# Performance work log

Hardware: AMD Instinct MI355X
Metric: run time of the kernel (lower is better)

The kernel has to match this reference:

```python
import jax, jax.numpy as jnp
import numpy as np
from jax import lax

B = 8192; LE = 40; LD = 12; PQ = 237; IN = PQ + 19; H = 64


def setup_inputs() -> dict:
    key = jax.random.key(0)
    ks = jax.random.split(key, 26)
    def n(k, shape, s=0.05):
        return jax.random.normal(k, shape, jnp.float32) * s
    return {
        "input_p_q": jax.random.normal(ks[0], (B, LE, PQ), jnp.float32),
        "label_p": jax.random.normal(ks[1], (B, LE), jnp.float32),
        "emb_hour": n(ks[2], (24, 5)),
        "emb_weekday": n(ks[3], (8, 3)),
        "emb_month": n(ks[4], (13, 4)),
        "emb_woy": n(ks[5], (54, 7)),
        "Wi_w": n(ks[6], (H, IN)), "Wi_b": n(ks[7], (H,)),
        "We_w": n(ks[8], (H, 2 * H)),
        "Vd_w": n(ks[9], (IN, H)), "Vd_b": n(ks[10], (IN,)),
        "enc_Wih": n(ks[11], (4 * H, IN)), "enc_Whh": n(ks[12], (4 * H, H)),
        "enc_bih": n(ks[13], (4 * H,)), "enc_bhh": n(ks[14], (4 * H,)),
        "Wd_w": n(ks[15], (H, H)), "Wd_b": n(ks[16], (H,)),
        "Wd2_w": n(ks[17], (H, 2)),
        "Vdt_w": n(ks[18], (1, H)), "Vdt_b": n(ks[19], (1,)),
        "dec_Wih": n(ks[20], (4, H + 1)), "dec_Whh": n(ks[21], (4, 1)),
        "dec_bih": n(ks[22], (4,)), "dec_bhh": n(ks[23], (4,)),
        "input_time": jax.random.randint(ks[24], (B, LE, 4), 0, 8),
        "decoder_time": jax.random.randint(ks[25], (B, LD), 0, 24),
    }


def _lstm_cell(x, h, c, Wih, Whh, bih, bhh):
    # PyTorch LSTMCell gate order: i, f, g, o
    g = x @ Wih.T + bih + h @ Whh.T + bhh
    i, f, gg, o = jnp.split(g, 4, axis=1)
    c = jax.nn.sigmoid(f) * c + jax.nn.sigmoid(i) * jnp.tanh(gg)
    h = jax.nn.sigmoid(o) * jnp.tanh(c)
    return h, c


def _forward(input_p_q, label_p, emb_hour, emb_weekday, emb_month, emb_woy,
             Wi_w, Wi_b, We_w, Vd_w, Vd_b,
             enc_Wih, enc_Whh, enc_bih, enc_bhh,
             Wd_w, Wd_b, Wd2_w, Vdt_w, Vdt_b,
             dec_Wih, dec_Whh, dec_bih, dec_bhh, input_time):
    b = input_p_q.shape[0]
    inputs = jnp.concatenate([
        input_p_q,
        emb_hour[input_time[:, :, 0]],
        emb_weekday[input_time[:, :, 1]],
        emb_month[input_time[:, :, 2]],
        emb_woy[input_time[:, :, 3]],
    ], axis=2)  # [B, LE, IN]

    def enc_step(carry, x_t):
        h, c = carry
        score = jnp.tanh(jnp.concatenate([h, c], 1) @ We_w.T
                         + x_t @ Wi_w.T + Wi_b) @ Vd_w.T + Vd_b  # [B, IN]
        x_in = x_t * jax.nn.softmax(score, axis=1)
        h, c = _lstm_cell(x_in, h, c, enc_Wih, enc_Whh, enc_bih, enc_bhh)
        return (h, c), h

    z = jnp.zeros((b, H), inputs.dtype)
    _, mid = lax.scan(enc_step, (z, z), jnp.swapaxes(inputs, 0, 1))
    mid_output = jnp.swapaxes(mid, 0, 1)  # [B, LE, H]

    wd_mid = mid_output @ Wd_w.T + Wd_b  # precompute Wd(mid_output), [B, LE, H]
    dec_p_in = label_p[:, LE - 1:LE]  # [B, 1], held constant across decode steps

    def dec_step(carry, _):
        hi, ci = carry  # [B, 1] each
        q = jnp.concatenate([hi, ci], 1) @ Wd2_w.T  # [B, H]
        score = jnp.tanh(q[:, None, :] + wd_mid) @ Vdt_w.T + Vdt_b  # [B, LE, 1] (no softmax, as in source)
        ctx = jnp.einsum('bt,btd->bd', score[..., 0], mid_output)  # [B, H]
        hi, ci = _lstm_cell(jnp.concatenate([ctx, dec_p_in], 1), hi, ci,
                            dec_Wih, dec_Whh, dec_bih, dec_bhh)
        return (hi, ci), hi

    z1 = jnp.zeros((b, 1), inputs.dtype)
    _, outs = lax.scan(dec_step, (z1, z1), None, length=LD)  # [LD, B, 1]
    return jnp.swapaxes(outs[..., 0], 0, 1)  # [B, LD]


def reference(input_p_q, label_p, emb_hour, emb_weekday, emb_month, emb_woy,
              Wi_w, Wi_b, We_w, Vd_w, Vd_b,
              enc_Wih, enc_Whh, enc_bih, enc_bhh,
              Wd_w, Wd_b, Wd2_w, Vdt_w, Vdt_b,
              dec_Wih, dec_Whh, dec_bih, dec_bhh, input_time, decoder_time):
    # decoder_time is accepted by the original forward but never used
    return _forward(input_p_q, label_p, emb_hour, emb_weekday, emb_month, emb_woy,
                    Wi_w, Wi_b, We_w, Vd_w, Vd_b,
                    enc_Wih, enc_Whh, enc_bih, enc_bhh,
                    Wd_w, Wd_b, Wd2_w, Vdt_w, Vdt_b,
                    dec_Wih, dec_Whh, dec_bih, dec_bhh, input_time)
```

## Files before the change

kernel.cpp:

```cpp
#include <hip/hip_runtime.h>

#define BB   8192
#define LEN  40
#define LDN  12
#define PQN  237
#define INN  256
#define HN   64
#define BT   32
#define ENC_BLOCKS (BB / BT)
#define DW   8
#define DEC_BLOCKS (BB / DW)
#define XPS  256

typedef unsigned int  u32;
typedef _Float16 f16;
typedef f16  half8 __attribute__((ext_vector_type(8)));
typedef f16  f16x4 __attribute__((ext_vector_type(4)));
typedef float f32x4 __attribute__((ext_vector_type(4)));

#define XS 264
#define HS 72

#define OFF_WI   0
#define OFF_WE   16384
#define OFF_VD   24576
#define OFF_WIH  40960
#define OFF_WHH  106496
#define OFF_WD   122880
#define W_TOTAL  126976

#define T_H   0
#define T_W   120
#define T_M   144
#define T_Y   196
#define T_TOT 574

#define PREP_BLOCKS (BB * LEN / 32)
#define CONV_BLOCKS ((W_TOTAL + 255) / 256)

__device__ __forceinline__ float rcp_(float x){
#if __has_builtin(__builtin_amdgcn_rcpf)
  return __builtin_amdgcn_rcpf(x);
#else
  return 1.0f / x;
#endif
}
__device__ __forceinline__ float sigm(float x){
  return rcp_(1.0f + exp2f(-1.44269504f * x));
}
__device__ __forceinline__ float tanhf_(float x){
  float e = exp2f(2.88539008f * x);
  return 1.0f - 2.0f * rcp_(e + 1.0f);
}

__device__ __forceinline__ void bar_lds(){
  asm volatile("s_waitcnt lgkmcnt(0)" ::: "memory");
  __builtin_amdgcn_s_barrier();
  asm volatile("" ::: "memory");
}

__global__ __launch_bounds__(256) void conv_w(
    const float* __restrict__ Wi, const float* __restrict__ We,
    const float* __restrict__ Vd, const float* __restrict__ Wih,
    const float* __restrict__ Whh, const float* __restrict__ Wd,
    f16* __restrict__ dst)
{
  int i = blockIdx.x * 256 + threadIdx.x;
  if (i >= W_TOTAL) return;
  float v;
  if      (i < OFF_WE)  v = Wi [i - OFF_WI ];
  else if (i < OFF_VD)  v = We [i - OFF_WE ];
  else if (i < OFF_WIH) v = Vd [i - OFF_VD ];
  else if (i < OFF_WHH) v = Wih[i - OFF_WIH];
  else if (i < OFF_WD)  v = Whh[i - OFF_WHH];
  else                  v = Wd [i - OFF_WD ];
  dst[i] = (f16)v;
}

__global__ __launch_bounds__(256) void prep_all(
    const float* __restrict__ ipq,
    const float* __restrict__ e_h, const float* __restrict__ e_w,
    const float* __restrict__ e_m, const float* __restrict__ e_y,
    const int*  __restrict__ itime,
    f16* __restrict__ xpre,
    const float* __restrict__ Wi, const float* __restrict__ We,
    const float* __restrict__ Vd, const float* __restrict__ Wih,
    const float* __restrict__ Whh, const float* __restrict__ Wd,
    f16* __restrict__ wdst)
{
  if (blockIdx.x >= PREP_BLOCKS) {
    int i = (blockIdx.x - PREP_BLOCKS) * 256 + threadIdx.x;
    if (i >= W_TOTAL) return;
    float v;
    if      (i < OFF_WE)  v = Wi [i - OFF_WI ];
    else if (i < OFF_VD)  v = We [i - OFF_WE ];
    else if (i < OFF_WIH) v = Vd [i - OFF_VD ];
    else if (i < OFF_WHH) v = Wih[i - OFF_WIH];
    else if (i < OFF_WD)  v = Whh[i - OFF_WHH];
    else                  v = Wd [i - OFF_WD ];
    wdst[i] = (f16)v;
    return;
  }
  const int wv = threadIdx.x >> 6, l = threadIdx.x & 63;
  const size_t row0 = (size_t)blockIdx.x * 32 + (size_t)wv * 8;
  int4 itv[8];
  #pragma unroll
  for (int r = 0; r < 8; ++r)
    itv[r] = *(const int4*)(itime + (row0 + r) * 4);
  #pragma unroll
  for (int r = 0; r < 8; ++r) {
    const size_t row = row0 + r;
    const float* src = ipq + row * PQN;
    f16* dst = xpre + row * XPS;
    #pragma unroll
    for (int k = 0; k < 3; ++k) {
      const int c = k * 64 + l;
      dst[c] = (f16)src[c];
    }
    {
      const int c = 192 + l;
      float v;
      if (c < PQN) v = src[c];
      else {
        const int o = c - PQN;
        if      (o < 5 ) v = e_h[itv[r].x * 5 + o];
        else if (o < 8 ) v = e_w[itv[r].y * 3 + (o - 5)];
        else if (o < 12) v = e_m[itv[r].z * 4 + (o - 8)];
        else             v = e_y[itv[r].w * 7 + (o - 12)];
      }
      dst[c] = (f16)v;
    }
  }
}

__global__ __launch_bounds__(512, 2) void enc_x(
    const f16* __restrict__ xpre,
    const float* __restrict__ Wi_b,
    const float* __restrict__ Vd_b,
    const float* __restrict__ ebih, const float* __restrict__ ebhh,
    const float* __restrict__ Wd_b,
    const f16*  __restrict__ wAll,
    f16* __restrict__ xout)
{
  __shared__ __attribute__((aligned(16))) f16 Xl[BT * XS];
  __shared__ __attribute__((aligned(16))) f16 Ul[BT * HS];
  __shared__ __attribute__((aligned(16))) f16 Hl[BT * HS];
  __shared__ __attribute__((aligned(16))) f16 Cl[BT * HS];
  __shared__ float Sred[2 * 64];
  __shared__ __attribute__((aligned(16))) f16 WiL[4 * 8 * 64 * 8];
  __shared__ __attribute__((aligned(16))) f16 WeL[4 * 4 * 64 * 8];
  __shared__ __attribute__((aligned(16))) f16 VdL[16 * 2 * 64 * 8];
  __shared__ __attribute__((aligned(16))) f16 WhL[16 * 2 * 64 * 8];
  __shared__ __attribute__((aligned(16))) f16 WdL[4 * 2 * 64 * 8];
  __shared__ float VdbL[256];
  __shared__ float EbsL[256];

  const int tid  = threadIdx.x;
  const int w    = tid >> 6;
  const int lane = tid & 63;
  const int nl   = lane & 15;
  const int q    = lane >> 4;
  const int wsub = w & 3;
  const int bt   = w >> 2;
  const int b0   = blockIdx.x * BT;
  const int d0   = wsub * 16 + q * 4;
  const int row  = bt * 16 + nl;

  const int r0  = tid >> 5;
  const int off = tid & 31;
  const f16* gb0 = xpre + ((size_t)(b0 + r0     ) * LEN) * XPS + off * 8;
  const f16* gb1 = xpre + ((size_t)(b0 + r0 + 16) * LEN) * XPS + off * 8;
  const u32 lwa = (u32)(r0 * XS + off * 8);
  const u32 lwb = (u32)((r0 + 16) * XS + off * 8);

  const int orow = tid >> 4;
  const int oc4  = (tid & 15) * 4;

  half8 sr0 = *(const half8*)gb0;
  half8 sr1 = *(const half8*)gb1;

  half8 whf[4][8];
  #pragma unroll
  for (int i = 0; i < 4; ++i) {
    const f16* ph = wAll + OFF_WIH + ((wsub + 4*i) * 16 + nl) * 256 + q * 8;
    #pragma unroll
    for (int kt = 0; kt < 8; ++kt) whf[i][kt] = *(const half8*)(ph + kt * 32);
  }
  float wib[4], wdb[4];
  #pragma unroll
  for (int r = 0; r < 4; ++r) { wib[r] = Wi_b[d0 + r]; wdb[r] = Wd_b[d0 + r]; }

  for (int s = tid; s < 4 * 8 * 64; s += 512) {
    const int tile = s >> 9, kt = (s >> 6) & 7, ln = s & 63;
    *(half8*)(&WiL[(size_t)s * 8]) = *(const half8*)(
        wAll + OFF_WI + (tile * 16 + (ln & 15)) * 256 + (ln >> 4) * 8 + kt * 32);
  }
  for (int s = tid; s < 4 * 4 * 64; s += 512) {
    const int tile = s >> 8, j = (s >> 6) & 3, ln = s & 63;
    *(half8*)(&WeL[(size_t)s * 8]) = *(const half8*)(
        wAll + OFF_WE + (tile * 16 + (ln & 15)) * 128 + (ln >> 4) * 8 + j * 32);
  }
  for (int s = tid; s < 16 * 2 * 64; s += 512) {
    const int tile = s >> 7, kt = (s >> 6) & 1, ln = s & 63;
    *(half8*)(&VdL[(size_t)s * 8]) = *(const half8*)(
        wAll + OFF_VD + (tile * 16 + (ln & 15)) * 64 + (ln >> 4) * 8 + kt * 32);
  }
  for (int s = tid; s < 16 * 2 * 64; s += 512) {
    const int tile = s >> 7, kt = (s >> 6) & 1, ln = s & 63;
    *(half8*)(&WhL[(size_t)s * 8]) = *(const half8*)(
        wAll + OFF_WHH + (tile * 16 + (ln & 15)) * 64 + (ln >> 4) * 8 + kt * 32);
  }
  for (int s = tid; s < 4 * 2 * 64; s += 512) {
    const int tile = s >> 7, kt = (s >> 6) & 1, ln = s & 63;
    *(half8*)(&WdL[(size_t)s * 8]) = *(const half8*)(
        wAll + OFF_WD + (tile * 16 + (ln & 15)) * 64 + (ln >> 4) * 8 + kt * 32);
  }
  if (tid < 256) {
    VdbL[tid] = Vd_b[tid];
    EbsL[tid] = ebih[tid] + ebhh[tid];
  }
  for (int i = tid; i < BT * HS; i += 512) {
    Hl[i] = (f16)0.f; Cl[i] = (f16)0.f;
  }
  float creg[4] = {0.f, 0.f, 0.f, 0.f};
  bar_lds();

  for (int t = 0; t < LEN; ++t) {
    *(half8*)(&Xl[lwa]) = sr0;
    *(half8*)(&Xl[lwb]) = sr1;
    if (t + 1 < LEN) {
      sr0 = *(const half8*)(gb0 + (size_t)(t + 1) * XPS);
      sr1 = *(const half8*)(gb1 + (size_t)(t + 1) * XPS);
    }
    bar_lds();

    {
      f32x4 a0 = {0.f, 0.f, 0.f, 0.f}, a1 = {0.f, 0.f, 0.f, 0.f};
      const f16* xb = &Xl[row * XS + q * 8];
      #pragma unroll
      for (int kt = 0; kt < 4; ++kt)
        a0 = __builtin_amdgcn_mfma_f32_16x16x32_f16(
            *(const half8*)(&WiL[((wsub * 8 + kt) * 64 + lane) * 8]),
            *(const half8*)(xb + kt * 32), a0, 0, 0, 0);
      #pragma unroll
      for (int kt = 4; kt < 8; ++kt)
        a1 = __builtin_amdgcn_mfma_f32_16x16x32_f16(
            *(const half8*)(&WiL[((wsub * 8 + kt) * 64 + lane) * 8]),
            *(const half8*)(xb + kt * 32), a1, 0, 0, 0);
      const f16* hb = &Hl[row * HS + q * 8];
      const f16* cb = &Cl[row * HS + q * 8];
      half8 h0 = *(const half8*)hb, h1 = *(const half8*)(hb + 32);
      half8 c0 = *(const half8*)cb, c1 = *(const half8*)(cb + 32);
      a0 = __builtin_amdgcn_mfma_f32_16x16x32_f16(
          *(const half8*)(&WeL[((wsub * 4 + 0) * 64 + lane) * 8]), h0, a0, 0, 0, 0);
      a1 = __builtin_amdgcn_mfma_f32_16x16x32_f16(
          *(const half8*)(&WeL[((wsub * 4 + 1) * 64 + lane) * 8]), h1, a1, 0, 0, 0);
      a0 = __builtin_amdgcn_mfma_f32_16x16x32_f16(
          *(const half8*)(&WeL[((wsub * 4 + 2) * 64 + lane) * 8]), c0, a0, 0, 0, 0);
      a1 = __builtin_amdgcn_mfma_f32_16x16x32_f16(
          *(const half8*)(&WeL[((wsub * 4 + 3) * 64 + lane) * 8]), c1, a1, 0, 0, 0);
      f16x4 uv;
      #pragma unroll
      for (int r = 0; r < 4; ++r) uv[r] = (f16)tanhf_(a0[r] + a1[r] + wib[r]);
      *(f16x4*)(&Ul[row * HS + d0]) = uv;
      if (t > 0) {
        f32x4 aw = {0.f, 0.f, 0.f, 0.f};
        aw = __builtin_amdgcn_mfma_f32_16x16x32_f16(
            *(const half8*)(&WdL[((wsub * 2 + 0) * 64 + lane) * 8]), h0, aw, 0, 0, 0);
        aw = __builtin_amdgcn_mfma_f32_16x16x32_f16(
            *(const half8*)(&WdL[((wsub * 2 + 1) * 64 + lane) * 8]), h1, aw, 0, 0, 0);
        f16x4 wv;
        #pragma unroll
        for (int r = 0; r < 4; ++r) wv[r] = (f16)(aw[r] + wdb[r]);
        *(f16x4*)(&xout[((size_t)(b0 + row) * LEN + (t - 1)) * XPS + 64 + d0]) = wv;
      }
    }
    bar_lds();

    if (t > 0) {
      f16x4 hv4 = *(const f16x4*)(&Hl[orow * HS + oc4]);
      *(f16x4*)(&xout[((size_t)(b0 + orow) * LEN + (t - 1)) * XPS + oc4]) = hv4;
    }
    {
      const f16* ub = &Ul[row * HS + q * 8];
      half8 u0 = *(const half8*)ub, u1 = *(const half8*)(ub + 32);
      float s = 0.f;
      #pragma unroll
      for (int i = 0; i < 4; ++i) {
        const int tile = wsub + 4 * i;
        f32x4 acc = {0.f, 0.f, 0.f, 0.f};
        acc = __builtin_amdgcn_mfma_f32_16x16x32_f16(
            *(const half8*)(&VdL[((tile * 2 + 0) * 64 + lane) * 8]), u0, acc, 0, 0, 0);
        acc = __builtin_amdgcn_mfma_f32_16x16x32_f16(
            *(const half8*)(&VdL[((tile * 2 + 1) * 64 + lane) * 8]), u1, acc, 0, 0, 0);
        const int k = tile * 16 + q * 4;
        f16x4 xv = *(const f16x4*)(&Xl[row * XS + k]);
        f16x4 pv;
        float ee[4];
        #pragma unroll
        for (int r = 0; r < 4; ++r) {
          ee[r] = exp2f((acc[r] + VdbL[k + r]) * 1.44269504f);
          s += ee[r];
          pv[r] = (f16)((float)xv[r] * ee[r]);
        }
        *(f16x4*)(&Xl[row * XS + k]) = pv;
      }
      s += __shfl_xor(s, 16, 64);
      s += __shfl_xor(s, 32, 64);
      if (lane < 16) Sred[bt * 64 + wsub * 16 + lane] = s;
    }
    bar_lds();

    f16x4 hv, cv;
    {
      f32x4 g[4], gh[4];
      #pragma unroll
      for (int i = 0; i < 4; ++i) {
        g[i]  = (f32x4){0.f, 0.f, 0.f, 0.f};
        gh[i] = (f32x4){0.f, 0.f, 0.f, 0.f};
      }
      const f16* pb = &Xl[row * XS + q * 8];
      #pragma unroll
      for (int kt = 0; kt < 8; ++kt) {
        half8 bv = *(const half8*)(pb + kt * 32);
        #pragma unroll
        for (int i = 0; i < 4; ++i)
          g[i] = __builtin_amdgcn_mfma_f32_16x16x32_f16(whf[i][kt], bv, g[i], 0, 0, 0);
      }
      const f16* hb = &Hl[row * HS + q * 8];
      half8 h0 = *(const half8*)hb, h1 = *(const half8*)(hb + 32);
      #pragma unroll
      for (int i = 0; i < 4; ++i) {
        const int tile = wsub + 4 * i;
        gh[i] = __builtin_amdgcn_mfma_f32_16x16x32_f16(
            *(const half8*)(&WhL[((tile * 2 + 0) * 64 + lane) * 8]), h0, gh[i], 0, 0, 0);
        gh[i] = __builtin_amdgcn_mfma_f32_16x16x32_f16(
            *(const half8*)(&WhL[((tile * 2 + 1) * 64 + lane) * 8]), h1, gh[i], 0, 0, 0);
      }
      const float inv = rcp_(Sred[bt*64 + nl]      + Sred[bt*64 + 16 + nl]
                           + Sred[bt*64 + 32 + nl] + Sred[bt*64 + 48 + nl]);
      #pragma unroll
      for (int r = 0; r < 4; ++r) {
        const float gi = g[0][r] * inv + gh[0][r] + EbsL[0   + d0 + r];
        const float gf = g[1][r] * inv + gh[1][r] + EbsL[64  + d0 + r];
        const float gg = g[2][r] * inv + gh[2][r] + EbsL[128 + d0 + r];
        const float go = g[3][r] * inv + gh[3][r] + EbsL[192 + d0 + r];
        float c = sigm(gf) * creg[r] + sigm(gi) * tanhf_(gg);
        creg[r] = c;
        const float h = sigm(go) * tanhf_(c);
        hv[r] = (f16)h; cv[r] = (f16)c;
      }
    }
    bar_lds();
    *(f16x4*)(&Hl[row * HS + d0]) = hv;
    *(f16x4*)(&Cl[row * HS + d0]) = cv;
  }

  bar_lds();
  {
    const f16* hb = &Hl[row * HS + q * 8];
    half8 h0 = *(const half8*)hb, h1 = *(const half8*)(hb + 32);
    f32x4 aw = {0.f, 0.f, 0.f, 0.f};
    aw = __builtin_amdgcn_mfma_f32_16x16x32_f16(
        *(const half8*)(&WdL[((wsub * 2 + 0) * 64 + lane) * 8]), h0, aw, 0, 0, 0);
    aw = __builtin_amdgcn_mfma_f32_16x16x32_f16(
        *(const half8*)(&WdL[((wsub * 2 + 1) * 64 + lane) * 8]), h1, aw, 0, 0, 0);
    f16x4 wv;
    #pragma unroll
    for (int r = 0; r < 4; ++r) wv[r] = (f16)(aw[r] + wdb[r]);
    *(f16x4*)(&xout[((size_t)(b0 + row) * LEN + (LEN - 1)) * XPS + 64 + d0]) = wv;
    f16x4 hv4 = *(const f16x4*)(&Hl[orow * HS + oc4]);
    *(f16x4*)(&xout[((size_t)(b0 + orow) * LEN + (LEN - 1)) * XPS + oc4]) = hv4;
  }
}

__global__ __launch_bounds__(256, 1) void enc_fb(
    const float* __restrict__ ipq,
    const float* __restrict__ e_h, const float* __restrict__ e_w,
    const float* __restrict__ e_m, const float* __restrict__ e_y,
    const float* __restrict__ Wi_b, const float* __restrict__ Vd_b,
    const float* __restrict__ ebih, const float* __restrict__ ebhh,
    const float* __restrict__ Wd_b, const f16* __restrict__ wAll,
    const int*  __restrict__ itime,
    f16* __restrict__ mid, f16* __restrict__ wmid)
{
  __shared__ __attribute__((aligned(16))) f16 Xl[BT * XS];
  __shared__ __attribute__((aligned(16))) f16 Ul[BT * HS];
  __shared__ __attribute__((aligned(16))) f16 Hl[BT * HS];
  __shared__ __attribute__((aligned(16))) f16 Cl[BT * HS];
  __shared__ float Sred[2 * 64];
  __shared__ float Tl[T_TOT];

  const int tid  = threadIdx.x;
  const int w    = tid >> 6;
  const int lane = tid & 63;
  const int nl   = lane & 15;
  const int q    = lane >> 4;
  const int b0   = blockIdx.x * BT;
  const int d0   = w * 16 + q * 4;

  const u32* pptr;
  int pstr, tstr, tbase = 0, twid = 0, tsub = 0;
  if (tid < PQN) {
    pptr = (const u32*)ipq + tid; pstr = LEN * PQN; tstr = PQN;
  } else {
    const int o = tid - PQN; int sel;
    if      (o < 5 ) { sel = 0; tbase = T_H; twid = 5; tsub = o;      }
    else if (o < 8 ) { sel = 1; tbase = T_W; twid = 3; tsub = o - 5;  }
    else if (o < 12) { sel = 2; tbase = T_M; twid = 4; tsub = o - 8;  }
    else             { sel = 3; tbase = T_Y; twid = 7; tsub = o - 12; }
    pptr = (const u32*)itime + sel; pstr = LEN * 4; tstr = 4;
  }
  pptr += (size_t)b0 * pstr;

  u32 pf[BT];
  #pragma unroll
  for (int bb = 0; bb < BT; ++bb) pf[bb] = pptr[(size_t)bb * pstr];

  half8 wif[8], wef[4], vdf[4][2], whf[4][8], whhf[4][2], wdf[2];
  {
    const f16* pw = wAll + OFF_WI + (w * 16 + nl) * 256 + q * 8;
    #pragma unroll
    for (int kt = 0; kt < 8; ++kt) wif[kt] = *(const half8*)(pw + kt * 32);
    const f16* pe = wAll + OFF_WE + (w * 16 + nl) * 128 + q * 8;
    #pragma unroll
    for (int kt = 0; kt < 4; ++kt) wef[kt] = *(const half8*)(pe + kt * 32);
    #pragma unroll
    for (int i = 0; i < 4; ++i) {
      const f16* pv = wAll + OFF_VD + ((w + 4*i) * 16 + nl) * 64 + q * 8;
      #pragma unroll
      for (int kt = 0; kt < 2; ++kt) vdf[i][kt] = *(const half8*)(pv + kt * 32);
      const f16* ph = wAll + OFF_WIH + ((w + 4*i) * 16 + nl) * 256 + q * 8;
      #pragma unroll
      for (int kt = 0; kt < 8; ++kt) whf[i][kt] = *(const half8*)(ph + kt * 32);
      const f16* pq = wAll + OFF_WHH + ((w + 4*i) * 16 + nl) * 64 + q * 8;
      #pragma unroll
      for (int kt = 0; kt < 2; ++kt) whhf[i][kt] = *(const half8*)(pq + kt * 32);
    }
    const f16* pd = wAll + OFF_WD + (w * 16 + nl) * 64 + q * 8;
    #pragma unroll
    for (int kt = 0; kt < 2; ++kt) wdf[kt] = *(const half8*)(pd + kt * 32);
  }

  float wib[4], vdb[16], ebs[16], wdb[4];
  #pragma unroll
  for (int r = 0; r < 4; ++r) { wib[r] = Wi_b[d0 + r]; wdb[r] = Wd_b[d0 + r]; }
  #pragma unroll
  for (int i = 0; i < 4; ++i)
    #pragma unroll
    for (int r = 0; r < 4; ++r) {
      vdb[i*4+r] = Vd_b[(w + 4*i) * 16 + q * 4 + r];
      ebs[i*4+r] = ebih[i * 64 + d0 + r] + ebhh[i * 64 + d0 + r];
    }

  for (int i = tid; i < BT * HS; i += 256) { Hl[i] = (f16)0.f; Cl[i] = (f16)0.f; }
  for (int i = tid; i < T_TOT; i += 256) {
    float v;
    if      (i < T_W) v = e_h[i];
    else if (i < T_M) v = e_w[i - T_W];
    else if (i < T_Y) v = e_m[i - T_M];
    else              v = e_y[i - T_Y];
    Tl[i] = v;
  }
  float creg[2][4];
  #pragma unroll
  for (int bt = 0; bt < 2; ++bt)
    #pragma unroll
    for (int r = 0; r < 4; ++r) creg[bt][r] = 0.f;
  bar_lds();

  for (int t = 0; t < LEN; ++t) {
    #pragma unroll
    for (int bb = 0; bb < BT; ++bb) {
      float v;
      if (tid < PQN) v = __uint_as_float(pf[bb]);
      else           v = Tl[tbase + (int)pf[bb] * twid + tsub];
      Xl[bb * XS + tid] = (f16)v;
    }
    if (t + 1 < LEN) {
      const u32* pp = pptr + (size_t)(t + 1) * tstr;
      #pragma unroll
      for (int bb = 0; bb < BT; ++bb) pf[bb] = pp[(size_t)bb * pstr];
    }
    bar_lds();

    #pragma unroll
    for (int bt = 0; bt < 2; ++bt) {
      const int row = bt * 16 + nl;
      f32x4 acc = {0.f, 0.f, 0.f, 0.f};
      const f16* xb = &Xl[row * XS + q * 8];
      #pragma unroll
      for (int kt = 0; kt < 8; ++kt)
        acc = __builtin_amdgcn_mfma_f32_16x16x32_f16(wif[kt], *(const half8*)(xb + kt * 32), acc, 0, 0, 0);
      const f16* hb = &Hl[row * HS + q * 8];
      const f16* cb = &Cl[row * HS + q * 8];
      half8 h0 = *(const half8*)hb, h1 = *(const half8*)(hb + 32);
      half8 c0 = *(const half8*)cb, c1 = *(const half8*)(cb + 32);
      acc = __builtin_amdgcn_mfma_f32_16x16x32_f16(wef[0], h0, acc, 0, 0, 0);
      acc = __builtin_amdgcn_mfma_f32_16x16x32_f16(wef[1], h1, acc, 0, 0, 0);
      acc = __builtin_amdgcn_mfma_f32_16x16x32_f16(wef[2], c0, acc, 0, 0, 0);
      acc = __builtin_amdgcn_mfma_f32_16x16x32_f16(wef[3], c1, acc, 0, 0, 0);
      f16x4 uv;
      #pragma unroll
      for (int r = 0; r < 4; ++r) uv[r] = (f16)tanhf_(acc[r] + wib[r]);
      *(f16x4*)(&Ul[row * HS + d0]) = uv;
      if (t > 0) {
        f32x4 aw = {0.f, 0.f, 0.f, 0.f};
        aw = __builtin_amdgcn_mfma_f32_16x16x32_f16(wdf[0], h0, aw, 0, 0, 0);
        aw = __builtin_amdgcn_mfma_f32_16x16x32_f16(wdf[1], h1, aw, 0, 0, 0);
        f16x4 wv;
        #pragma unroll
        for (int r = 0; r < 4; ++r) wv[r] = (f16)(aw[r] + wdb[r]);
        *(f16x4*)(&wmid[((size_t)(b0 + row) * LEN + (t - 1)) * HN + d0]) = wv;
      }
    }
    bar_lds();

    #pragma unroll
    for (int bt = 0; bt < 2; ++bt) {
      const int row = bt * 16 + nl;
      const f16* ub = &Ul[row * HS + q * 8];
      half8 u0 = *(const half8*)ub, u1 = *(const half8*)(ub + 32);
      float ee[16];
      #pragma unroll
      for (int i = 0; i < 4; ++i) {
        f32x4 acc = {0.f, 0.f, 0.f, 0.f};
        acc = __builtin_amdgcn_mfma_f32_16x16x32_f16(vdf[i][0], u0, acc, 0, 0, 0);
        acc = __builtin_amdgcn_mfma_f32_16x16x32_f16(vdf[i][1], u1, acc, 0, 0, 0);
        #pragma unroll
        for (int r = 0; r < 4; ++r)
          ee[i*4+r] = exp2f((acc[r] + vdb[i*4+r]) * 1.44269504f);
      }
      float s = 0.f;
      #pragma unroll
      for (int j = 0; j < 16; ++j) s += ee[j];
      s += __shfl_xor(s, 16, 64);
      s += __shfl_xor(s, 32, 64);
      if (lane < 16) Sred[bt * 64 + w * 16 + lane] = s;
      #pragma unroll
      for (int i = 0; i < 4; ++i) {
        const int k = (w + 4*i) * 16 + q * 4;
        f16x4 xv = *(const f16x4*)(&Xl[row * XS + k]);
        f16x4 pv;
        #pragma unroll
        for (int r = 0; r < 4; ++r) pv[r] = (f16)((float)xv[r] * ee[i*4+r]);
        *(f16x4*)(&Xl[row * XS + k]) = pv;
      }
    }
    bar_lds();

    f16x4 hstash[2], cstash[2];
    #pragma unroll
    for (int bt = 0; bt < 2; ++bt) {
      const int row = bt * 16 + nl;
      f32x4 g[4], gh[4];
      #pragma unroll
      for (int i = 0; i < 4; ++i) {
        g[i]  = (f32x4){0.f, 0.f, 0.f, 0.f};
        gh[i] = (f32x4){0.f, 0.f, 0.f, 0.f};
      }
      const f16* pb = &Xl[row * XS + q * 8];
      #pragma unroll
      for (int kt = 0; kt < 8; ++kt) {
        half8 bv = *(const half8*)(pb + kt * 32);
        #pragma unroll
        for (int i = 0; i < 4; ++i)
          g[i] = __builtin_amdgcn_mfma_f32_16x16x32_f16(whf[i][kt], bv, g[i], 0, 0, 0);
      }
      const f16* hb = &Hl[row * HS + q * 8];
      half8 h0 = *(const half8*)hb, h1 = *(const half8*)(hb + 32);
      #pragma unroll
      for (int i = 0; i < 4; ++i) {
        gh[i] = __builtin_amdgcn_mfma_f32_16x16x32_f16(whhf[i][0], h0, gh[i], 0, 0, 0);
        gh[i] = __builtin_amdgcn_mfma_f32_16x16x32_f16(whhf[i][1], h1, gh[i], 0, 0, 0);
      }
      const float inv = rcp_(Sred[bt*64 + nl]      + Sred[bt*64 + 16 + nl]
                           + Sred[bt*64 + 32 + nl] + Sred[bt*64 + 48 + nl]);
      f16x4 hv, cv;
      #pragma unroll
      for (int r = 0; r < 4; ++r) {
        const float gi = g[0][r] * inv + gh[0][r] + ebs[0  + r];
        const float gf = g[1][r] * inv + gh[1][r] + ebs[4  + r];
        const float gg = g[2][r] * inv + gh[2][r] + ebs[8  + r];
        const float go = g[3][r] * inv + gh[3][r] + ebs[12 + r];
        float c = sigm(gf) * creg[bt][r] + sigm(gi) * tanhf_(gg);
        creg[bt][r] = c;
        const float h = sigm(go) * tanhf_(c);
        hv[r] = (f16)h; cv[r] = (f16)c;
      }
      hstash[bt] = hv; cstash[bt] = cv;
      *(f16x4*)(&mid[((size_t)(b0 + row) * LEN + t) * HN + d0]) = hv;
    }
    bar_lds();
    #pragma unroll
    for (int bt = 0; bt < 2; ++bt) {
      const int row = bt * 16 + nl;
      *(f16x4*)(&Hl[row * HS + d0]) = hstash[bt];
      *(f16x4*)(&Cl[row * HS + d0]) = cstash[bt];
    }
  }

  bar_lds();
  #pragma unroll
  for (int bt = 0; bt < 2; ++bt) {
    const int row = bt * 16 + nl;
    const f16* hb = &Hl[row * HS + q * 8];
    half8 h0 = *(const half8*)hb, h1 = *(const half8*)(hb + 32);
    f32x4 aw = {0.f, 0.f, 0.f, 0.f};
    aw = __builtin_amdgcn_mfma_f32_16x16x32_f16(wdf[0], h0, aw, 0, 0, 0);
    aw = __builtin_amdgcn_mfma_f32_16x16x32_f16(wdf[1], h1, aw, 0, 0, 0);
    f16x4 wv;
    #pragma unroll
    for (int r = 0; r < 4; ++r) wv[r] = (f16)(aw[r] + wdb[r]);
    *(f16x4*)(&wmid[((size_t)(b0 + row) * LEN + (LEN - 1)) * HN + d0]) = wv;
  }
}

__global__ __launch_bounds__(512) void dec_kernel(
    const f16* __restrict__ mids,
    const f16* __restrict__ wms,
    const int MS,
    const float* __restrict__ lblp,
    const float* __restrict__ Wd2_w,
    const float* __restrict__ Vdt_w,
    const float* __restrict__ Vdt_b,
    const float* __restrict__ dWih,
    const float* __restrict__ dWhh,
    const float* __restrict__ dbih, const float* __restrict__ dbhh,
    float* __restrict__ out)
{
  __shared__ __attribute__((aligned(16))) float qv[DW][HN];
  __shared__ __attribute__((aligned(16))) float vs[HN];
  __shared__ __attribute__((aligned(16))) float ws4[4 * 65];

  const int w    = threadIdx.x >> 6;
  const int lane = threadIdx.x & 63;
  const int b    = blockIdx.x * DW + w;

  if (threadIdx.x < HN)     vs[threadIdx.x]  = Vdt_w[threadIdx.x];
  if (threadIdx.x < 4 * 65) ws4[threadIdx.x] = dWih[threadIdx.x];

  half8 wmr[8];
  if (lane < LEN) {
    const f16* p = wms + ((size_t)b * LEN + lane) * MS;
    #pragma unroll
    for (int k = 0; k < 8; ++k) wmr[k] = *(const half8*)(p + k * 8);
  } else {
    #pragma unroll
    for (int k = 0; k < 8; ++k)
      #pragma unroll
      for (int e = 0; e < 8; ++e) wmr[k][e] = (f16)0.f;
  }
  __syncthreads();

  float macc[4] = {0.f, 0.f, 0.f, 0.f};
  if (lane < LEN) {
    const f16* mrow = mids + ((size_t)b * LEN + lane) * MS;
    #pragma unroll
    for (int k8 = 0; k8 < 8; ++k8) {
      half8 mv = *(const half8*)(mrow + k8 * 8);
      #pragma unroll
      for (int e = 0; e < 8; ++e) {
        const float m = (float)mv[e];
        #pragma unroll
        for (int j = 0; j < 4; ++j) macc[j] += ws4[j * 65 + k8 * 8 + e] * m;
      }
    }
  }

  const float dpin = lblp[b * LEN + (LEN - 1)];
  const float w20 = Wd2_w[2 * lane];
  const float w21 = Wd2_w[2 * lane + 1];
  const float vdtb = Vdt_b[0];
  float wxx[4], whh4[4], bb4[4];
  #pragma unroll
  for (int j = 0; j < 4; ++j) {
    wxx[j]  = dWih[j * 65 + 64];
    whh4[j] = dWhh[j];
    bb4[j]  = dbih[j] + dbhh[j];
  }

  float hi = 0.0f, ci = 0.0f;
  for (int s = 0; s < LDN; ++s) {
    qv[w][lane] = w20 * hi + w21 * ci;

    float p0 = 0.f, p1 = 0.f, p2 = 0.f, p3 = 0.f;
    if (lane < LEN) {
      float acc = 0.f;
      #pragma unroll
      for (int k8 = 0; k8 < 8; ++k8) {
        float4 qa = *(const float4*)&qv[w][k8 * 8];
        float4 qb = *(const float4*)&qv[w][k8 * 8 + 4];
        float4 va = *(const float4*)&vs[k8 * 8];
        float4 vb = *(const float4*)&vs[k8 * 8 + 4];
        half8 wv = wmr[k8];
        acc += tanhf_(qa.x + (float)wv[0]) * va.x
             + tanhf_(qa.y + (float)wv[1]) * va.y
             + tanhf_(qa.z + (float)wv[2]) * va.z
             + tanhf_(qa.w + (float)wv[3]) * va.w
             + tanhf_(qb.x + (float)wv[4]) * vb.x
             + tanhf_(qb.y + (float)wv[5]) * vb.y
             + tanhf_(qb.z + (float)wv[6]) * vb.z
             + tanhf_(qb.w + (float)wv[7]) * vb.w;
      }
      const float score = acc + vdtb;
      p0 = score * macc[0]; p1 = score * macc[1];
      p2 = score * macc[2]; p3 = score * macc[3];
    }
    #pragma unroll
    for (int off = 32; off >= 1; off >>= 1) {
      p0 += __shfl_xor(p0, off, 64);
      p1 += __shfl_xor(p1, off, 64);
      p2 += __shfl_xor(p2, off, 64);
      p3 += __shfl_xor(p3, off, 64);
    }
    const float g0 = p0 + wxx[0] * dpin + bb4[0] + whh4[0] * hi;
    const float g1 = p1 + wxx[1] * dpin + bb4[1] + whh4[1] * hi;
    const float g2 = p2 + wxx[2] * dpin + bb4[2] + whh4[2] * hi;
    const float g3 = p3 + wxx[3] * dpin + bb4[3] + whh4[3] * hi;
    ci = sigm(g1) * ci + sigm(g0) * tanhf_(g2);
    hi = sigm(g3) * tanhf_(ci);
    if (lane == 0) out[b * LDN + s] = hi;
  }
}

extern "C" void kernel_launch(void* const* d_in, const int* in_sizes, int n_in,
                              void* d_out, int out_size, void* d_ws, size_t ws_size,
                              hipStream_t stream) {
  (void)in_sizes; (void)n_in; (void)out_size;
  const float* ipq   = (const float*)d_in[0];
  const float* lblp  = (const float*)d_in[1];
  const float* e_h   = (const float*)d_in[2];
  const float* e_w   = (const float*)d_in[3];
  const float* e_m   = (const float*)d_in[4];
  const float* e_y   = (const float*)d_in[5];
  const float* Wi_w  = (const float*)d_in[6];
  const float* Wi_b  = (const float*)d_in[7];
  const float* We_w  = (const float*)d_in[8];
  const float* Vd_w  = (const float*)d_in[9];
  const float* Vd_b  = (const float*)d_in[10];
  const float* eWih  = (const float*)d_in[11];
  const float* eWhh  = (const float*)d_in[12];
  const float* ebih  = (const float*)d_in[13];
  const float* ebhh  = (const float*)d_in[14];
  const float* Wd_w  = (const float*)d_in[15];
  const float* Wd_b  = (const float*)d_in[16];
  const float* Wd2_w = (const float*)d_in[17];
  const float* Vdt_w = (const float*)d_in[18];
  const float* Vdt_b = (const float*)d_in[19];
  const float* dWih  = (const float*)d_in[20];
  const float* dWhh  = (const float*)d_in[21];
  const float* dbih  = (const float*)d_in[22];
  const float* dbhh  = (const float*)d_in[23];
  const int* itime   = (const int*)d_in[24];
  float* out = (float*)d_out;

  const size_t xpreB = (size_t)BB * LEN * XPS * 2;
  const size_t wcvtB = (size_t)W_TOTAL * 2;

  if (ws_size >= xpreB + wcvtB) {
    f16* xpre = (f16*)d_ws;
    f16* wcvt = (f16*)((char*)d_ws + xpreB);
    prep_all<<<dim3(PREP_BLOCKS + CONV_BLOCKS), dim3(256), 0, stream>>>(
        ipq, e_h, e_w, e_m, e_y, itime, xpre,
        Wi_w, We_w, Vd_w, eWih, eWhh, Wd_w, wcvt);
    enc_x<<<dim3(ENC_BLOCKS), dim3(512), 0, stream>>>(
        xpre, Wi_b, Vd_b, ebih, ebhh, Wd_b, wcvt, xpre);
    dec_kernel<<<dim3(DEC_BLOCKS), dim3(512), 0, stream>>>(
        xpre, xpre + 64, XPS, lblp, Wd2_w, Vdt_w, Vdt_b,
        dWih, dWhh, dbih, dbhh, out);
  } else {
    const size_t midB = (size_t)BB * LEN * HN * 2;
    f16* mid  = (f16*)d_ws;
    f16* wmid = (f16*)((char*)d_ws + midB);
    f16* wcvt = (f16*)((char*)d_ws + 2 * midB);
    conv_w<<<dim3(CONV_BLOCKS), dim3(256), 0, stream>>>(
        Wi_w, We_w, Vd_w, eWih, eWhh, Wd_w, wcvt);
    enc_fb<<<dim3(ENC_BLOCKS), dim3(256), 0, stream>>>(
        ipq, e_h, e_w, e_m, e_y, Wi_b, Vd_b, ebih, ebhh, Wd_b, wcvt, itime,
        mid, wmid);
    dec_kernel<<<dim3(DEC_BLOCKS), dim3(512), 0, stream>>>(
        mid, wmid, HN, lblp, Wd2_w, Vdt_w, Vdt_b,
        dWih, dWhh, dbih, dbhh, out);
  }
}
```

Measured before the change: 828.8 us.

## Transpose decoder attention so lanes own hidden dims and loop over timesteps

The decoder kernel now gives each lane one hidden dimension and loops over the 40 encoder timesteps, instead of giving each lane one timestep and looping over 64 dims. Before, 24 of 64 lanes sat idle. Per-timestep projected mid outputs are staged in shared memory, and the constant Vdt_b contribution is folded into a per-gate constant computed once. This removes the per-step shared-memory write of the query vector and uses all lanes for the tanh work. In exchange it adds 40 strided f16 loads per lane and a 40-float register array, which raises register pressure.

```diff
diff --git a/kernel.cpp b/kernel.cpp
--- a/kernel.cpp
+++ b/kernel.cpp
@@ -629,28 +629,19 @@
     const float* __restrict__ dbih, const float* __restrict__ dbhh,
     float* __restrict__ out)
 {
-  __shared__ __attribute__((aligned(16))) float qv[DW][HN];
-  __shared__ __attribute__((aligned(16))) float vs[HN];
+  __shared__ __attribute__((aligned(16))) float M4L[DW][LEN][4];
   __shared__ __attribute__((aligned(16))) float ws4[4 * 65];
 
   const int w    = threadIdx.x >> 6;
   const int lane = threadIdx.x & 63;
   const int b    = blockIdx.x * DW + w;
 
-  if (threadIdx.x < HN)     vs[threadIdx.x]  = Vdt_w[threadIdx.x];
+  float wcol[LEN];
+  #pragma unroll
+  for (int t = 0; t < LEN; ++t)
+    wcol[t] = (float)wms[((size_t)b * LEN + t) * MS + lane];
+
   if (threadIdx.x < 4 * 65) ws4[threadIdx.x] = dWih[threadIdx.x];
-
-  half8 wmr[8];
-  if (lane < LEN) {
-    const f16* p = wms + ((size_t)b * LEN + lane) * MS;
-    #pragma unroll
-    for (int k = 0; k < 8; ++k) wmr[k] = *(const half8*)(p + k * 8);
-  } else {
-    #pragma unroll
-    for (int k = 0; k < 8; ++k)
-      #pragma unroll
-      for (int e = 0; e < 8; ++e) wmr[k][e] = (f16)0.f;
-  }
   __syncthreads();
 
   float macc[4] = {0.f, 0.f, 0.f, 0.f};
@@ -667,57 +658,52 @@
       }
     }
   }
+  float sm4[4];
+  #pragma unroll
+  for (int j = 0; j < 4; ++j) {
+    float p = macc[j];
+    #pragma unroll
+    for (int off = 32; off >= 1; off >>= 1) p += __shfl_xor(p, off, 64);
+    sm4[j] = p;
+  }
+  if (lane < LEN) {
+    M4L[w][lane][0] = macc[0]; M4L[w][lane][1] = macc[1];
+    M4L[w][lane][2] = macc[2]; M4L[w][lane][3] = macc[3];
+  }
 
   const float dpin = lblp[b * LEN + (LEN - 1)];
-  const float w20 = Wd2_w[2 * lane];
-  const float w21 = Wd2_w[2 * lane + 1];
+  const float w20  = Wd2_w[2 * lane];
+  const float w21  = Wd2_w[2 * lane + 1];
+  const float v    = Vdt_w[lane];
   const float vdtb = Vdt_b[0];
-  float wxx[4], whh4[4], bb4[4];
+  float cj[4], whh4[4];
   #pragma unroll
   for (int j = 0; j < 4; ++j) {
-    wxx[j]  = dWih[j * 65 + 64];
     whh4[j] = dWhh[j];
-    bb4[j]  = dbih[j] + dbhh[j];
+    cj[j] = dWih[j * 65 + 64] * dpin + dbih[j] + dbhh[j] + vdtb * sm4[j];
   }
 
   float hi = 0.0f, ci = 0.0f;
   for (int s = 0; s < LDN; ++s) {
-    qv[w][lane] = w20 * hi + w21 * ci;
-
-    float p0 = 0.f, p1 = 0.f, p2 = 0.f, p3 = 0.f;
-    if (lane < LEN) {
-      float acc = 0.f;
-      #pragma unroll
-      for (int k8 = 0; k8 < 8; ++k8) {
-        float4 qa = *(const float4*)&qv[w][k8 * 8];
-        float4 qb = *(const float4*)&qv[w][k8 * 8 + 4];
-        float4 va = *(const float4*)&vs[k8 * 8];
-        float4 vb = *(const float4*)&vs[k8 * 8 + 4];
-        half8 wv = wmr[k8];
-        acc += tanhf_(qa.x + (float)wv[0]) * va.x
-             + tanhf_(qa.y + (float)wv[1]) * va.y
-             + tanhf_(qa.z + (float)wv[2]) * va.z
-             + tanhf_(qa.w + (float)wv[3]) * va.w
-             + tanhf_(qb.x + (float)wv[4]) * vb.x
-             + tanhf_(qb.y + (float)wv[5]) * vb.y
-             + tanhf_(qb.z + (float)wv[6]) * vb.z
-             + tanhf_(qb.w + (float)wv[7]) * vb.w;
-      }
-      const float score = acc + vdtb;
-      p0 = score * macc[0]; p1 = score * macc[1];
-      p2 = score * macc[2]; p3 = score * macc[3];
+    const float q = w20 * hi + w21 * ci;
+    float a0 = 0.f, a1 = 0.f, a2 = 0.f, a3 = 0.f;
+    #pragma unroll
+    for (int t = 0; t < LEN; ++t) {
+      const float p = v * tanhf_(q + wcol[t]);
+      const float4 m4 = *(const float4*)&M4L[w][t][0];
+      a0 += p * m4.x; a1 += p * m4.y; a2 += p * m4.z; a3 += p * m4.w;
     }
     #pragma unroll
     for (int off = 32; off >= 1; off >>= 1) {
-      p0 += __shfl_xor(p0, off, 64);
-      p1 += __shfl_xor(p1, off, 64);
-      p2 += __shfl_xor(p2, off, 64);
-      p3 += __shfl_xor(p3, off, 64);
-    }
-    const float g0 = p0 + wxx[0] * dpin + bb4[0] + whh4[0] * hi;
-    const float g1 = p1 + wxx[1] * dpin + bb4[1] + whh4[1] * hi;
-    const float g2 = p2 + wxx[2] * dpin + bb4[2] + whh4[2] * hi;
-    const float g3 = p3 + wxx[3] * dpin + bb4[3] + whh4[3] * hi;
+      a0 += __shfl_xor(a0, off, 64);
+      a1 += __shfl_xor(a1, off, 64);
+      a2 += __shfl_xor(a2, off, 64);
+      a3 += __shfl_xor(a3, off, 64);
+    }
+    const float g0 = a0 + cj[0] + whh4[0] * hi;
+    const float g1 = a1 + cj[1] + whh4[1] * hi;
+    const float g2 = a2 + cj[2] + whh4[2] * hi;
+    const float g3 = a3 + cj[3] + whh4[3] * hi;
     ci = sigm(g1) * ci + sigm(g0) * tanhf_(g2);
     hi = sigm(g3) * tanhf_(ci);
     if (lane == 0) out[b * LDN + s] = hi;
```

Measured after the change: 802.3 us. 1.03x faster.
